# Kernel optimization log

Measured on AMD Instinct MI355X. Metric: run time of the kernel, lower is better.

Reference implementation:

```python
import jax, jax.numpy as jnp
import numpy as np

N = 100000
E = 1600000
F_IN, H, C = 128, 128, 64


def setup_inputs() -> dict:
    key = jax.random.key(0)
    ks = jax.random.split(key, 8)
    x = jax.random.normal(ks[0], (N, F_IN), dtype=jnp.float32)
    edge_index = jax.random.randint(ks[1], (2, E), 0, N, dtype=jnp.int64)
    s = lambda fi: (1.0 / np.sqrt(fi))
    # SAGEConv1: lin_l (applied to mean-aggregated neighbors, has bias), lin_r (root, no bias)
    W1l = jax.random.uniform(ks[2], (H, F_IN), jnp.float32, -s(F_IN), s(F_IN))
    b1 = jnp.zeros((H,), jnp.float32)
    W1r = jax.random.uniform(ks[3], (H, F_IN), jnp.float32, -s(F_IN), s(F_IN))
    # SAGEConv2
    W2l = jax.random.uniform(ks[4], (C, H), jnp.float32, -s(H), s(H))
    b2 = jnp.zeros((C,), jnp.float32)
    W2r = jax.random.uniform(ks[5], (C, H), jnp.float32, -s(H), s(H))
    return {"x": x, "edge_index": edge_index, "W1l": W1l, "b1": b1, "W1r": W1r,
            "W2l": W2l, "b2": b2, "W2r": W2r}


def _mean_aggr(x, src, dst):
    # mean over incoming neighbors (PyG flow: edge_index[0]=source -> edge_index[1]=target)
    msg = x[src]                                            # [E, F] big gather
    summed = jax.ops.segment_sum(msg, dst, num_segments=N)  # [N, F]
    cnt = jax.ops.segment_sum(jnp.ones((src.shape[0],), x.dtype), dst, num_segments=N)
    return summed / jnp.clip(cnt, 1.0)[:, None]


def _sage_conv(x, src, dst, Wl, b, Wr):
    agg = _mean_aggr(x, src, dst)
    return agg @ Wl.T + b + x @ Wr.T


def _iconv(x, src, dst):
    # weight-free GCN propagation: D^-1/2 (A + I) D^-1/2 @ x
    loops = jnp.arange(N, dtype=src.dtype)
    s2 = jnp.concatenate([src, loops])
    d2 = jnp.concatenate([dst, loops])
    deg = jax.ops.segment_sum(jnp.ones((s2.shape[0],), x.dtype), d2, num_segments=N)
    dis = jnp.where(deg > 0, jax.lax.rsqrt(jnp.maximum(deg, 1.0)), 0.0)
    norm = dis[s2] * dis[d2]                               # [E+N]
    return jax.ops.segment_sum(norm[:, None] * x[s2], d2, num_segments=N)


def reference(x, edge_index, W1l, b1, W1r, W2l, b2, W2r):
    src, dst = edge_index[0], edge_index[1]
    h = jax.nn.relu(_sage_conv(x, src, dst, W1l, b1, W1r))
    # F.dropout(training=False) -> identity in eval mode
    h = _sage_conv(h, src, dst, W2l, b2, W2r)
    return _iconv(h, src, dst)
```

## Files before the change

### kernel.cpp

```cpp
#include <hip/hip_runtime.h>

#define GN 100000
#define GE 1600000
#define GF 128
#define GH 128
#define GC 64

#define NB 392
#define SLABSZ 5376
#define P1_EDGES 4096
#define P1_BLOCKS ((GE + P1_EDGES - 1) / P1_EDGES)
#define CASTX_BLOCKS 12500

typedef __attribute__((ext_vector_type(8))) short v8s;
typedef __attribute__((ext_vector_type(4))) float v4f;

__device__ __forceinline__ unsigned short f2bf(float f) {
    union { float f; unsigned u; } a; a.f = f;
    unsigned r = a.u + 0x7fff + ((a.u >> 16) & 1);
    return (unsigned short)(r >> 16);
}
__device__ __forceinline__ float bf2f(unsigned short b) {
    union { unsigned u; float f; } a; a.u = ((unsigned)b) << 16;
    return a.f;
}

__global__ __launch_bounds__(256) void prep_kernel(
    unsigned* __restrict__ slab, int* __restrict__ bucket_cnt,
    const int* __restrict__ src, const int* __restrict__ dst,
    unsigned short* __restrict__ xb, const float* __restrict__ x,
    unsigned short* w1l, unsigned short* w1r,
    unsigned short* w2l, unsigned short* w2r,
    const float* W1l, const float* W1r,
    const float* W2l, const float* W2r)
{
    __shared__ int hist[512];
    __shared__ int scanex[512];
    __shared__ int cursor[512];
    __shared__ int gbase[512];
    __shared__ int ssum[256];
    __shared__ unsigned stage[P1_EDGES];
    __shared__ unsigned short sbid[P1_EDGES];

    int tid = threadIdx.x;
    int blk = blockIdx.x;

    if (blk >= P1_BLOCKS) {
        int cb = blk - P1_BLOCKS;
        if (cb < CASTX_BLOCKS) {
            int i = cb * 256 + tid;
            float4 v = ((const float4*)x)[i];
            ushort4 u;
            u.x = f2bf(v.x); u.y = f2bf(v.y); u.z = f2bf(v.z); u.w = f2bf(v.w);
            ((ushort4*)xb)[i] = u;
            return;
        }
        int i = (cb - CASTX_BLOCKS) * 256 + tid;
        const float* s; unsigned short* d; int off;
        if      (i <  4096) { s = W1l; d = w1l; off = i; }
        else if (i <  8192) { s = W1r; d = w1r; off = i - 4096; }
        else if (i < 10240) { s = W2l; d = w2l; off = i - 8192; }
        else if (i < 12288) { s = W2r; d = w2r; off = i - 10240; }
        else return;
        float4 v = ((const float4*)s)[off];
        ushort4 u;
        u.x = f2bf(v.x); u.y = f2bf(v.y); u.z = f2bf(v.z); u.w = f2bf(v.w);
        ((ushort4*)d)[off] = u;
        return;
    }

    int e0 = blk * P1_EDGES;
    int nE = min(P1_EDGES, GE - e0);

    unsigned pk[16]; int bk[16];
    hist[tid] = 0; hist[tid + 256] = 0;
    __syncthreads();
    #pragma unroll
    for (int j = 0; j < 16; ++j) {
        int i = j * 256 + tid;
        if (i < nE) {
            int e = e0 + i;
            int d = dst[e], s = src[e];
            int b = d >> 8;
            pk[j] = ((unsigned)(d & 255) << 17) | (unsigned)s;
            bk[j] = b;
            atomicAdd(&hist[b], 1);
        } else bk[j] = -1;
    }
    __syncthreads();
    int a0 = hist[2 * tid], a1 = hist[2 * tid + 1];
    int s2 = a0 + a1;
    ssum[tid] = s2;
    __syncthreads();
    for (int off = 1; off < 256; off <<= 1) {
        int v = (tid >= off) ? ssum[tid - off] : 0;
        __syncthreads();
        ssum[tid] += v;
        __syncthreads();
    }
    int pbase = ssum[tid] - s2;
    scanex[2 * tid] = pbase;          cursor[2 * tid] = pbase;
    scanex[2 * tid + 1] = pbase + a0; cursor[2 * tid + 1] = pbase + a0;
    __syncthreads();
    #pragma unroll
    for (int j = 0; j < 16; ++j) {
        if (bk[j] >= 0) {
            int pos = atomicAdd(&cursor[bk[j]], 1);
            stage[pos] = pk[j];
            sbid[pos] = (unsigned short)bk[j];
        }
    }
    for (int b = tid; b < NB; b += 256) {
        int c = hist[b];
        gbase[b] = c ? atomicAdd(&bucket_cnt[b], c) : 0;
    }
    __syncthreads();
    for (int i = tid; i < nE; i += 256) {
        int b = sbid[i];
        int go = gbase[b] + (i - scanex[b]);
        if (go < SLABSZ)
            slab[(size_t)b * SLABSZ + go] = stage[i];
    }
}

__global__ __launch_bounds__(256) void bucket_pass2_kernel(
    int* __restrict__ csr, int* __restrict__ row_ptr,
    float* __restrict__ invc, float* __restrict__ dis,
    const unsigned* __restrict__ slab, const int* __restrict__ bucket_cnt)
{
    __shared__ int deg_l[256];
    __shared__ int excl[256];
    __shared__ int cur[256];
    __shared__ int ssum[256];
    __shared__ int bstart_s;
    __shared__ unsigned stage[SLABSZ];

    int t = threadIdx.x;
    int b = blockIdx.x;

    int c0 = (2 * t < NB) ? bucket_cnt[2 * t] : 0;
    int c1 = (2 * t + 1 < NB) ? bucket_cnt[2 * t + 1] : 0;
    int sc = c0 + c1;
    ssum[t] = sc;
    __syncthreads();
    for (int off = 1; off < 256; off <<= 1) {
        int v = (t >= off) ? ssum[t - off] : 0;
        __syncthreads();
        ssum[t] += v;
        __syncthreads();
    }
    int pb = ssum[t] - sc;
    if (2 * t == b)     bstart_s = pb;
    if (2 * t + 1 == b) bstart_s = pb + c0;
    if (b == NB - 1 && t == 0) row_ptr[GN] = GE;

    int cnt = min(bucket_cnt[b], SLABSZ);
    const unsigned* sp = slab + (size_t)b * SLABSZ;
    deg_l[t] = 0;
    __syncthreads();
    int base = bstart_s;
    for (int i = t; i < cnt; i += 256)
        atomicAdd(&deg_l[sp[i] >> 17], 1);
    __syncthreads();
    int dg = deg_l[t];
    ssum[t] = dg;
    __syncthreads();
    for (int off = 1; off < 256; off <<= 1) {
        int v = (t >= off) ? ssum[t - off] : 0;
        __syncthreads();
        ssum[t] += v;
        __syncthreads();
    }
    int ex = ssum[t] - dg;
    excl[t] = ex; cur[t] = ex;
    __syncthreads();
    int d = b * 256 + t;
    if (d < GN) {
        row_ptr[d] = base + ex;
        float c = (float)dg;
        invc[d] = 1.0f / fmaxf(c, 1.0f);
        dis[d] = rsqrtf(c + 1.0f);
    }
    for (int i = t; i < cnt; i += 256) {
        unsigned p = sp[i];
        int pos = atomicAdd(&cur[p >> 17], 1);
        stage[pos] = p & 0x1FFFFu;
    }
    __syncthreads();
    for (int i = t; i < cnt; i += 256)
        csr[base + i] = (int)stage[i];
}

__global__ __launch_bounds__(256) void dual_gemm_kernel(
    unsigned short* __restrict__ C,
    const unsigned short* __restrict__ A1, const unsigned short* __restrict__ A2,
    const unsigned short* __restrict__ W1, const unsigned short* __restrict__ W2,
    const float* __restrict__ bias, int M)
{
    int tid = threadIdx.x;
    int wv = tid >> 6, lane = tid & 63;
    int lm = lane & 15, quad = lane >> 4;
    int m_base = blockIdx.x * 256 + wv * 64;

    for (int nh = 0; nh < 2; ++nh) {
        int n_base = nh * 64;
        v4f acc[4][4];
        #pragma unroll
        for (int mt = 0; mt < 4; ++mt)
            #pragma unroll
            for (int nt = 0; nt < 4; ++nt) acc[mt][nt] = (v4f){0.f,0.f,0.f,0.f};

        #pragma unroll
        for (int ks = 0; ks < 4; ++ks) {
            int koff = ks * 32 + quad * 8;
            v8s a1[4], a2[4], b1[4], b2[4];
            #pragma unroll
            for (int mt = 0; mt < 4; ++mt) {
                int row = m_base + mt * 16 + lm;
                if (row < M) {
                    a1[mt] = *(const v8s*)(A1 + (size_t)row * 128 + koff);
                    a2[mt] = *(const v8s*)(A2 + (size_t)row * 128 + koff);
                } else {
                    a1[mt] = (v8s){0,0,0,0,0,0,0,0};
                    a2[mt] = (v8s){0,0,0,0,0,0,0,0};
                }
            }
            #pragma unroll
            for (int nt = 0; nt < 4; ++nt) {
                int col = n_base + nt * 16 + lm;
                b1[nt] = *(const v8s*)(W1 + (size_t)col * 128 + koff);
                b2[nt] = *(const v8s*)(W2 + (size_t)col * 128 + koff);
            }
            #pragma unroll
            for (int mt = 0; mt < 4; ++mt)
                #pragma unroll
                for (int nt = 0; nt < 4; ++nt) {
                    acc[mt][nt] = __builtin_amdgcn_mfma_f32_16x16x32_bf16(a1[mt], b1[nt], acc[mt][nt], 0, 0, 0);
                    acc[mt][nt] = __builtin_amdgcn_mfma_f32_16x16x32_bf16(a2[mt], b2[nt], acc[mt][nt], 0, 0, 0);
                }
        }

        #pragma unroll
        for (int mt = 0; mt < 4; ++mt)
            #pragma unroll
            for (int r = 0; r < 4; ++r) {
                int row = m_base + mt * 16 + quad * 4 + r;
                if (row >= M) continue;
                #pragma unroll
                for (int nt = 0; nt < 4; ++nt) {
                    int col = n_base + nt * 16 + lm;
                    float v = acc[mt][nt][r] + bias[col];
                    v = fmaxf(v, 0.f);
                    C[(size_t)row * 128 + col] = f2bf(v);
                }
            }
    }
}

__global__ __launch_bounds__(256) void gemm64_dual_kernel(
    unsigned short* __restrict__ P, unsigned short* __restrict__ Q,
    const unsigned short* __restrict__ A,
    const unsigned short* __restrict__ Wl, const unsigned short* __restrict__ Wr,
    const float* __restrict__ b2, int M)
{
    int tid = threadIdx.x;
    int wv = tid >> 6, lane = tid & 63;
    int lm = lane & 15, quad = lane >> 4;
    int m_base = blockIdx.x * 256 + wv * 64;

    v4f accP[4][4], accQ[4][4];
    #pragma unroll
    for (int mt = 0; mt < 4; ++mt)
        #pragma unroll
        for (int nt = 0; nt < 4; ++nt) {
            accP[mt][nt] = (v4f){0.f,0.f,0.f,0.f};
            accQ[mt][nt] = (v4f){0.f,0.f,0.f,0.f};
        }

    #pragma unroll
    for (int ks = 0; ks < 4; ++ks) {
        int koff = ks * 32 + quad * 8;
        v8s af[4], bl[4], br[4];
        #pragma unroll
        for (int mt = 0; mt < 4; ++mt) {
            int row = m_base + mt * 16 + lm;
            if (row < M) af[mt] = *(const v8s*)(A + (size_t)row * 128 + koff);
            else         af[mt] = (v8s){0,0,0,0,0,0,0,0};
        }
        #pragma unroll
        for (int nt = 0; nt < 4; ++nt) {
            int col = nt * 16 + lm;
            bl[nt] = *(const v8s*)(Wl + (size_t)col * 128 + koff);
            br[nt] = *(const v8s*)(Wr + (size_t)col * 128 + koff);
        }
        #pragma unroll
        for (int mt = 0; mt < 4; ++mt)
            #pragma unroll
            for (int nt = 0; nt < 4; ++nt) {
                accP[mt][nt] = __builtin_amdgcn_mfma_f32_16x16x32_bf16(af[mt], bl[nt], accP[mt][nt], 0, 0, 0);
                accQ[mt][nt] = __builtin_amdgcn_mfma_f32_16x16x32_bf16(af[mt], br[nt], accQ[mt][nt], 0, 0, 0);
            }
    }

    #pragma unroll
    for (int mt = 0; mt < 4; ++mt)
        #pragma unroll
        for (int r = 0; r < 4; ++r) {
            int row = m_base + mt * 16 + quad * 4 + r;
            if (row >= M) continue;
            #pragma unroll
            for (int nt = 0; nt < 4; ++nt) {
                int col = nt * 16 + lm;
                P[(size_t)row * 64 + col] = f2bf(accP[mt][nt][r]);
                Q[(size_t)row * 64 + col] = f2bf(accQ[mt][nt][r] + b2[col]);
            }
        }
}

__global__ __launch_bounds__(256) void gather_mean128_kernel(
    unsigned short* __restrict__ out, const unsigned short* __restrict__ in,
    const float* __restrict__ invc, const int* __restrict__ row_ptr,
    const int* __restrict__ csr, int N)
{
    int wid = (blockIdx.x * 256 + threadIdx.x) >> 6;
    int lane = threadIdx.x & 63;
    if (wid >= N) return;
    int half = lane >> 5, k = lane & 31;
    int beg = row_ptr[wid], end = row_ptr[wid + 1];
    float ax = 0.f, ay = 0.f, az = 0.f, aw = 0.f;
    int j = beg + half;
    for (; j + 6 < end; j += 8) {
        int s0 = csr[j], s1 = csr[j + 2], s2 = csr[j + 4], s3 = csr[j + 6];
        ushort4 a = ((const ushort4*)(in + (size_t)s0 * 128))[k];
        ushort4 b = ((const ushort4*)(in + (size_t)s1 * 128))[k];
        ushort4 c = ((const ushort4*)(in + (size_t)s2 * 128))[k];
        ushort4 d = ((const ushort4*)(in + (size_t)s3 * 128))[k];
        ax += (bf2f(a.x) + bf2f(b.x)) + (bf2f(c.x) + bf2f(d.x));
        ay += (bf2f(a.y) + bf2f(b.y)) + (bf2f(c.y) + bf2f(d.y));
        az += (bf2f(a.z) + bf2f(b.z)) + (bf2f(c.z) + bf2f(d.z));
        aw += (bf2f(a.w) + bf2f(b.w)) + (bf2f(c.w) + bf2f(d.w));
    }
    for (; j < end; j += 2) {
        ushort4 a = ((const ushort4*)(in + (size_t)csr[j] * 128))[k];
        ax += bf2f(a.x); ay += bf2f(a.y); az += bf2f(a.z); aw += bf2f(a.w);
    }
    ax += __shfl_xor(ax, 32); ay += __shfl_xor(ay, 32);
    az += __shfl_xor(az, 32); aw += __shfl_xor(aw, 32);
    if (half == 0) {
        float ic = invc[wid];
        ushort4 o;
        o.x = f2bf(ax * ic); o.y = f2bf(ay * ic);
        o.z = f2bf(az * ic); o.w = f2bf(aw * ic);
        ((ushort4*)(out + (size_t)wid * 128))[k] = o;
    }
}

__global__ __launch_bounds__(256) void gather_combine_kernel(
    unsigned short* __restrict__ h2s, const unsigned short* __restrict__ p,
    const unsigned short* __restrict__ q,
    const float* __restrict__ invc, const float* __restrict__ dis,
    const int* __restrict__ row_ptr, const int* __restrict__ csr, int N)
{
    int wid = (blockIdx.x * 256 + threadIdx.x) >> 6;
    int lane = threadIdx.x & 63;
    if (wid >= N) return;
    int half = lane >> 5, k = lane & 31;
    int beg = row_ptr[wid], end = row_ptr[wid + 1];
    float ax = 0.f, ay = 0.f;
    int j = beg + half;
    for (; j + 6 < end; j += 8) {
        int s0 = csr[j], s1 = csr[j + 2], s2 = csr[j + 4], s3 = csr[j + 6];
        unsigned a = ((const unsigned*)(p + (size_t)s0 * 64))[k];
        unsigned b = ((const unsigned*)(p + (size_t)s1 * 64))[k];
        unsigned c = ((const unsigned*)(p + (size_t)s2 * 64))[k];
        unsigned d = ((const unsigned*)(p + (size_t)s3 * 64))[k];
        ax += (bf2f((unsigned short)(a & 0xffff)) + bf2f((unsigned short)(b & 0xffff)))
            + (bf2f((unsigned short)(c & 0xffff)) + bf2f((unsigned short)(d & 0xffff)));
        ay += (bf2f((unsigned short)(a >> 16)) + bf2f((unsigned short)(b >> 16)))
            + (bf2f((unsigned short)(c >> 16)) + bf2f((unsigned short)(d >> 16)));
    }
    for (; j < end; j += 2) {
        unsigned a = ((const unsigned*)(p + (size_t)csr[j] * 64))[k];
        ax += bf2f((unsigned short)(a & 0xffff));
        ay += bf2f((unsigned short)(a >> 16));
    }
    ax += __shfl_xor(ax, 32); ay += __shfl_xor(ay, 32);
    if (half == 0) {
        float ic = invc[wid], dd = dis[wid];
        unsigned qv = ((const unsigned*)(q + (size_t)wid * 64))[k];
        float ox = dd * (ax * ic + bf2f((unsigned short)(qv & 0xffff)));
        float oy = dd * (ay * ic + bf2f((unsigned short)(qv >> 16)));
        unsigned o = (unsigned)f2bf(ox) | ((unsigned)f2bf(oy) << 16);
        ((unsigned*)(h2s + (size_t)wid * 64))[k] = o;
    }
}

__global__ __launch_bounds__(256) void iconv_kernel(
    float* __restrict__ out, const unsigned short* __restrict__ h2s,
    const float* __restrict__ dis, const int* __restrict__ row_ptr,
    const int* __restrict__ csr, int N)
{
    int wid = (blockIdx.x * 256 + threadIdx.x) >> 6;
    int lane = threadIdx.x & 63;
    if (wid >= N) return;
    int half = lane >> 5, k = lane & 31;
    int beg = row_ptr[wid], end = row_ptr[wid + 1];
    float ax = 0.f, ay = 0.f;
    int j = beg + half;
    for (; j + 6 < end; j += 8) {
        int s0 = csr[j], s1 = csr[j + 2], s2 = csr[j + 4], s3 = csr[j + 6];
        unsigned a = ((const unsigned*)(h2s + (size_t)s0 * 64))[k];
        unsigned b = ((const unsigned*)(h2s + (size_t)s1 * 64))[k];
        unsigned c = ((const unsigned*)(h2s + (size_t)s2 * 64))[k];
        unsigned d = ((const unsigned*)(h2s + (size_t)s3 * 64))[k];
        ax += (bf2f((unsigned short)(a & 0xffff)) + bf2f((unsigned short)(b & 0xffff)))
            + (bf2f((unsigned short)(c & 0xffff)) + bf2f((unsigned short)(d & 0xffff)));
        ay += (bf2f((unsigned short)(a >> 16)) + bf2f((unsigned short)(b >> 16)))
            + (bf2f((unsigned short)(c >> 16)) + bf2f((unsigned short)(d >> 16)));
    }
    for (; j < end; j += 2) {
        unsigned a = ((const unsigned*)(h2s + (size_t)csr[j] * 64))[k];
        ax += bf2f((unsigned short)(a & 0xffff));
        ay += bf2f((unsigned short)(a >> 16));
    }
    ax += __shfl_xor(ax, 32); ay += __shfl_xor(ay, 32);
    if (half == 0) {
        unsigned s = ((const unsigned*)(h2s + (size_t)wid * 64))[k];
        ax += bf2f((unsigned short)(s & 0xffff));
        ay += bf2f((unsigned short)(s >> 16));
        float dd = dis[wid];
        ((float2*)(out + (size_t)wid * 64))[k] = make_float2(dd * ax, dd * ay);
    }
}

extern "C" void kernel_launch(void* const* d_in, const int* in_sizes, int n_in,
                              void* d_out, int out_size, void* d_ws, size_t ws_size,
                              hipStream_t stream) {
    const float* x   = (const float*)d_in[0];
    const int*   ei  = (const int*)d_in[1];
    const float* W1l = (const float*)d_in[2];
    const float* b1  = (const float*)d_in[3];
    const float* W1r = (const float*)d_in[4];
    const float* W2l = (const float*)d_in[5];
    const float* b2  = (const float*)d_in[6];
    const float* W2r = (const float*)d_in[7];
    float* out = (float*)d_out;

    const int* src = ei;
    const int* dst = ei + GE;

    float* invc = (float*)d_ws;
    float* dis  = invc + GN;
    unsigned short* regA = (unsigned short*)(dis + GN);
    unsigned short* regB = regA + (size_t)GN * 128;
    unsigned short* regC = regB + (size_t)GN * 128;
    unsigned short* xb    = regA;
    unsigned short* aggx  = regB;
    unsigned short* hb    = regC;
    unsigned short* pb    = regA;
    unsigned short* qb    = regA + (size_t)GN * 64;
    unsigned short* h2s   = regB;
    unsigned short* w1lb = regC + (size_t)GN * 128;
    unsigned short* w1rb = w1lb + GH * GF;
    unsigned short* w2lb = w1rb + GH * GF;
    unsigned short* w2rb = w2lb + GC * GH;
    int* row_ptr      = (int*)(w2rb + GC * GH);
    int* bucket_cnt   = row_ptr + GN + 1;
    unsigned* slab    = (unsigned*)(bucket_cnt + NB);
    int* csr          = (int*)(slab + (size_t)NB * SLABSZ);

    const int T = 256;
    const int g_wave = (GN * 64 + T - 1) / T;
    dim3 g_dual((GN + 255) / 256, 1);
    dim3 g_g64((GN + 255) / 256, 1);

    hipMemsetAsync(bucket_cnt, 0, NB * sizeof(int), stream);
    prep_kernel<<<P1_BLOCKS + CASTX_BLOCKS + 48, T, 0, stream>>>(
        slab, bucket_cnt, src, dst,
        xb, x, w1lb, w1rb, w2lb, w2rb, W1l, W1r, W2l, W2r);

    bucket_pass2_kernel<<<NB, T, 0, stream>>>(csr, row_ptr, invc, dis,
                                              slab, bucket_cnt);

    gather_mean128_kernel<<<g_wave, T, 0, stream>>>(aggx, xb, invc, row_ptr, csr, GN);
    dual_gemm_kernel<<<g_dual, T, 0, stream>>>(hb, aggx, xb, w1lb, w1rb, b1, GN);

    gemm64_dual_kernel<<<g_g64, T, 0, stream>>>(pb, qb, hb, w2lb, w2rb, b2, GN);
    gather_combine_kernel<<<g_wave, T, 0, stream>>>(h2s, pb, qb, invc, dis,
                                                    row_ptr, csr, GN);

    iconv_kernel<<<g_wave, T, 0, stream>>>(out, h2s, dis, row_ptr, csr, GN);
}
```

Baseline: 388.6 us.

## Fuse layer-1 and layer-2 GEMMs, keeping hidden activations in LDS

Merges the first SAGE dual GEMM (bias+ReLU) and the second layer's dual projection GEMM into one kernel. The 256x128 bf16 hidden tile is staged in shared memory instead of being written to and re-read from global memory. This removes one launch and a full N x 128 bf16 round trip. In exchange it uses about 68KB of LDS per block, which may cut occupancy, adds a block-wide barrier, and moves the P/Q buffers to a new workspace region after the CSR.

```diff
diff --git a/kernel.cpp b/kernel.cpp
--- a/kernel.cpp
+++ b/kernel.cpp
@@ -191,16 +191,20 @@
         csr[base + i] = (int)stage[i];
 }
 
-__global__ __launch_bounds__(256) void dual_gemm_kernel(
-    unsigned short* __restrict__ C,
+__global__ __launch_bounds__(256) void fused_gemm_kernel(
+    unsigned short* __restrict__ P, unsigned short* __restrict__ Q,
     const unsigned short* __restrict__ A1, const unsigned short* __restrict__ A2,
     const unsigned short* __restrict__ W1, const unsigned short* __restrict__ W2,
-    const float* __restrict__ bias, int M)
-{
+    const unsigned short* __restrict__ Wl, const unsigned short* __restrict__ Wr,
+    const float* __restrict__ b1, const float* __restrict__ b2, int M)
+{
+    __shared__ unsigned short hs[256][136];
+
     int tid = threadIdx.x;
     int wv = tid >> 6, lane = tid & 63;
     int lm = lane & 15, quad = lane >> 4;
     int m_base = blockIdx.x * 256 + wv * 64;
+    int row_l0 = wv * 64;
 
     for (int nh = 0; nh < 2; ++nh) {
         int n_base = nh * 64;
@@ -213,7 +217,7 @@
         #pragma unroll
         for (int ks = 0; ks < 4; ++ks) {
             int koff = ks * 32 + quad * 8;
-            v8s a1[4], a2[4], b1[4], b2[4];
+            v8s a1[4], a2[4], bw1[4], bw2[4];
             #pragma unroll
             for (int mt = 0; mt < 4; ++mt) {
                 int row = m_base + mt * 16 + lm;
@@ -228,15 +232,15 @@
             #pragma unroll
             for (int nt = 0; nt < 4; ++nt) {
                 int col = n_base + nt * 16 + lm;
-                b1[nt] = *(const v8s*)(W1 + (size_t)col * 128 + koff);
-                b2[nt] = *(const v8s*)(W2 + (size_t)col * 128 + koff);
+                bw1[nt] = *(const v8s*)(W1 + (size_t)col * 128 + koff);
+                bw2[nt] = *(const v8s*)(W2 + (size_t)col * 128 + koff);
             }
             #pragma unroll
             for (int mt = 0; mt < 4; ++mt)
                 #pragma unroll
                 for (int nt = 0; nt < 4; ++nt) {
-                    acc[mt][nt] = __builtin_amdgcn_mfma_f32_16x16x32_bf16(a1[mt], b1[nt], acc[mt][nt], 0, 0, 0);
-                    acc[mt][nt] = __builtin_amdgcn_mfma_f32_16x16x32_bf16(a2[mt], b2[nt], acc[mt][nt], 0, 0, 0);
+                    acc[mt][nt] = __builtin_amdgcn_mfma_f32_16x16x32_bf16(a1[mt], bw1[nt], acc[mt][nt], 0, 0, 0);
+                    acc[mt][nt] = __builtin_amdgcn_mfma_f32_16x16x32_bf16(a2[mt], bw2[nt], acc[mt][nt], 0, 0, 0);
                 }
         }
 
@@ -244,29 +248,16 @@
         for (int mt = 0; mt < 4; ++mt)
             #pragma unroll
             for (int r = 0; r < 4; ++r) {
-                int row = m_base + mt * 16 + quad * 4 + r;
-                if (row >= M) continue;
+                int rl = row_l0 + mt * 16 + quad * 4 + r;
                 #pragma unroll
                 for (int nt = 0; nt < 4; ++nt) {
                     int col = n_base + nt * 16 + lm;
-                    float v = acc[mt][nt][r] + bias[col];
-                    v = fmaxf(v, 0.f);
-                    C[(size_t)row * 128 + col] = f2bf(v);
+                    float v = acc[mt][nt][r] + b1[col];
+                    hs[rl][col] = f2bf(fmaxf(v, 0.f));
                 }
             }
     }
-}
-
-__global__ __launch_bounds__(256) void gemm64_dual_kernel(
-    unsigned short* __restrict__ P, unsigned short* __restrict__ Q,
-    const unsigned short* __restrict__ A,
-    const unsigned short* __restrict__ Wl, const unsigned short* __restrict__ Wr,
-    const float* __restrict__ b2, int M)
-{
-    int tid = threadIdx.x;
-    int wv = tid >> 6, lane = tid & 63;
-    int lm = lane & 15, quad = lane >> 4;
-    int m_base = blockIdx.x * 256 + wv * 64;
+    __syncthreads();
 
     v4f accP[4][4], accQ[4][4];
     #pragma unroll
@@ -282,11 +273,8 @@
         int koff = ks * 32 + quad * 8;
         v8s af[4], bl[4], br[4];
         #pragma unroll
-        for (int mt = 0; mt < 4; ++mt) {
-            int row = m_base + mt * 16 + lm;
-            if (row < M) af[mt] = *(const v8s*)(A + (size_t)row * 128 + koff);
-            else         af[mt] = (v8s){0,0,0,0,0,0,0,0};
-        }
+        for (int mt = 0; mt < 4; ++mt)
+            af[mt] = *(const v8s*)&hs[row_l0 + mt * 16 + lm][koff];
         #pragma unroll
         for (int nt = 0; nt < 4; ++nt) {
             int col = nt * 16 + lm;
@@ -453,14 +441,12 @@
     float* dis  = invc + GN;
     unsigned short* regA = (unsigned short*)(dis + GN);
     unsigned short* regB = regA + (size_t)GN * 128;
-    unsigned short* regC = regB + (size_t)GN * 128;
     unsigned short* xb    = regA;
     unsigned short* aggx  = regB;
-    unsigned short* hb    = regC;
-    unsigned short* pb    = regA;
-    unsigned short* qb    = regA + (size_t)GN * 64;
-    unsigned short* h2s   = regB;
-    unsigned short* w1lb = regC + (size_t)GN * 128;
+    unsigned short* pb    = regB;
+    unsigned short* qb    = regB + (size_t)GN * 64;
+    unsigned short* h2s   = regA;
+    unsigned short* w1lb = regB + (size_t)GN * 128;
     unsigned short* w1rb = w1lb + GH * GF;
     unsigned short* w2lb = w1rb + GH * GF;
     unsigned short* w2rb = w2lb + GC * GH;
@@ -469,10 +455,14 @@
     unsigned* slab    = (unsigned*)(bucket_cnt + NB);
     int* csr          = (int*)(slab + (size_t)NB * SLABSZ);
 
+    unsigned short* pq = (unsigned short*)(csr + GE);
+    pb = pq;
+    qb = pq + (size_t)GN * 64;
+    h2s = regB;
+
     const int T = 256;
     const int g_wave = (GN * 64 + T - 1) / T;
-    dim3 g_dual((GN + 255) / 256, 1);
-    dim3 g_g64((GN + 255) / 256, 1);
+    dim3 g_fused((GN + 255) / 256, 1);
 
     hipMemsetAsync(bucket_cnt, 0, NB * sizeof(int), stream);
     prep_kernel<<<P1_BLOCKS + CASTX_BLOCKS + 48, T, 0, stream>>>(
@@ -483,9 +473,11 @@
                                               slab, bucket_cnt);
 
     gather_mean128_kernel<<<g_wave, T, 0, stream>>>(aggx, xb, invc, row_ptr, csr, GN);
-    dual_gemm_kernel<<<g_dual, T, 0, stream>>>(hb, aggx, xb, w1lb, w1rb, b1, GN);
-
-    gemm64_dual_kernel<<<g_g64, T, 0, stream>>>(pb, qb, hb, w2lb, w2rb, b2, GN);
+
+    fused_gemm_kernel<<<g_fused, T, 0, stream>>>(pb, qb, aggx, xb,
+                                                 w1lb, w1rb, w2lb, w2rb,
+                                                 b1, b2, GN);
+
     gather_combine_kernel<<<g_wave, T, 0, stream>>>(h2s, pb, qb, invc, dis,
                                                     row_ptr, csr, GN);
 
```

Result: no change. 387.2 us (-0.3%).
